# Performance work log

Measured on AMD Instinct MI355X. Metric: run time of the kernel, lower is better.

The kernel has to match this reference:

```python
import jax, jax.numpy as jnp
import numpy as np

B, J, Q, O, H1, H2 = 16384, 12, 7, 5, 128, 128


def _xavier(key, shape):
    fan_in, fan_out = shape[-2], shape[-1]
    limit = float(np.sqrt(6.0 / (fan_in + fan_out)))
    return jax.random.uniform(key, shape, jnp.float32, -limit, limit)


def setup_inputs() -> dict:
    key = jax.random.key(0)
    ks = jax.random.split(key, 8)
    x = jax.random.uniform(ks[0], (B, Q, O), jnp.float32)
    judge_ids = jax.random.randint(ks[1], (B,), 0, J, jnp.int64)
    return {
        "x": x,
        "judge_ids": judge_ids,
        "W1": _xavier(ks[2], (Q, O + 1, H1)),
        "W1_a": _xavier(ks[3], (J, Q, O + 1, H1)),
        "W2": _xavier(ks[4], (H1 + 1, H2)),
        "W2_a": _xavier(ks[5], (J, H1 + 1, H2)),
        "V": _xavier(ks[6], (Q, H2 + 1, O)),
        "V_a": _xavier(ks[7], (J, Q, H2 + 1, O)),
    }


def reference(x, judge_ids, W1, W1_a, W2, W2_a, V, V_a):
    b, q, _ = x.shape
    ones = jnp.ones((b, q, 1), x.dtype)
    # layer 1: per-(judge, question) weights with bias concat
    x_bias = jnp.concatenate([ones, x], axis=2)            # [b,q,O+1]
    W1c = W1[None] + W1_a[judge_ids]                        # [b,q,O+1,H1]
    z1 = jax.nn.sigmoid(jnp.einsum('bqi,bqih->bqh', x_bias, W1c))
    # layer 2: per-judge weights shared across questions
    z1_bias = jnp.concatenate([ones, z1], axis=2)           # [b,q,H1+1]
    W2c = W2[None] + W2_a[judge_ids]                        # [b,H1+1,H2]
    z2 = jax.nn.sigmoid(jnp.einsum('bqi,bih->bqh', z1_bias, W2c))
    # output layer: per-(judge, question) weights -> softmax over options
    z2_bias = jnp.concatenate([ones, z2], axis=2)           # [b,q,H2+1]
    Vc = V[None] + V_a[judge_ids]                           # [b,q,H2+1,O]
    logits = jnp.einsum('bqi,bqio->bqo', z2_bias, Vc)
    return jax.nn.softmax(logits, axis=-1)                  # [b,q,O]
```

## Files before the change

kernel.cpp:

```cpp
#include <hip/hip_runtime.h>
#include <hip/hip_bf16.h>

#define B_TOT 16384
#define NQ 7
#define NO 5

typedef float v4f __attribute__((ext_vector_type(4)));
typedef _Float16 v8h __attribute__((ext_vector_type(8)));

#define WS_W1F  0
#define WS_W2F  (WS_W1F + 49152)
#define WS_V3F  (WS_W2F + 98304)
#define WS_W2L  (WS_V3F + 86016)
#define WS_V3L  (WS_W2L + 1536)
#define WS_PERM (WS_V3L + 1344)
#define WS_HIST (WS_PERM + 12*16384)
#define WS_ISB  (WS_HIST + 768)
#define WS_TOT_U32 (WS_ISB + 1)
#define WS_NEEDED_BYTES ((size_t)WS_TOT_U32 * 4)

#define CFRAG_TOT (49152 + 98304 + 86016 + 1536 + 1344)
#define NBLK_COMBINE ((CFRAG_TOT + 255) / 256)
#define NBLK_SCATTER 64
#define NBLK_PRE (NBLK_COMBINE + NBLK_SCATTER)

__device__ __forceinline__ float ldf(const float* p) { return *p; }
__device__ __forceinline__ float ldf(const __hip_bfloat16* p) { return __bfloat162float(*p); }
__device__ __forceinline__ float sigmoidf_(float v) { return 1.0f / (1.0f + __expf(-v)); }
__device__ __forceinline__ unsigned short f2h(float f) {
    _Float16 h = (_Float16)f; return __builtin_bit_cast(unsigned short, h);
}
__device__ __forceinline__ float h2f(unsigned short u) {
    return (float)__builtin_bit_cast(_Float16, u);
}
__device__ __forceinline__ unsigned pack2(float a, float b) {
    return (unsigned)f2h(a) | ((unsigned)f2h(b) << 16);
}
__device__ __forceinline__ v8h bc8h(uint4 u) { return __builtin_bit_cast(v8h, u); }

__device__ __forceinline__ int probe_is_bf16(const unsigned int* w1bits) {
    int hits = 0;
    for (int t = 0; t < 64; ++t) {
        unsigned lo = w1bits[t] & 0xFFFFu, e = (lo >> 7) & 0xFFu;
        if (lo == 0u || (e >= 100u && e <= 130u)) ++hits;
    }
    return hits >= 32;
}
__device__ __forceinline__ int probe_is_j64(const int* jid) {
    int o = 0;
    for (int t = 0; t < 64; ++t) o |= jid[2*t + 1];
    return (o == 0) ? 1 : 0;
}

template<typename T>
__device__ __forceinline__ void combine_body(
    int idx, const T* W1, const T* W1a, const T* W2, const T* W2a,
    const T* V, const T* Va, unsigned* ws32, float* wsF)
{
    if (idx < 49152) {
        int p = idx & 3, l = (idx >> 2) & 63, nt = (idx >> 8) & 7,
            ks = (idx >> 11) & 1, j = idx >> 12;
        int n = nt*16 + (l & 15);
        float v[2];
        #pragma unroll
        for (int s = 0; s < 2; ++s) {
            int k = ks*32 + ((l >> 4) << 3) + 2*p + s;
            v[s] = (k < 42) ? (ldf(W1 + k*128 + n) + ldf(W1a + j*5376 + k*128 + n)) : 0.0f;
        }
        ws32[WS_W1F + idx] = pack2(v[0], v[1]);
    } else if (idx < 49152 + 98304) {
        int t = idx - 49152;
        int p = t & 3, l = (t >> 2) & 63, nt = (t >> 8) & 7,
            ks = (t >> 11) & 3, j = t >> 13;
        int n = nt*16 + (l & 15);
        float v[2];
        #pragma unroll
        for (int s = 0; s < 2; ++s) {
            int k = ks*32 + ((l >> 4) << 3) + 2*p + s;
            v[s] = ldf(W2 + k*128 + n) + ldf(W2a + (j*129 + k)*128 + n);
        }
        ws32[WS_W2F + t] = pack2(v[0], v[1]);
    } else if (idx < 49152 + 98304 + 86016) {
        int t = idx - (49152 + 98304);
        int p = t & 3, l = (t >> 2) & 63, ks = (t >> 8) & 3;
        int jq = t >> 10, q = jq % 7, j = jq / 7;
        int n = l & 15;
        float v[2];
        #pragma unroll
        for (int s = 0; s < 2; ++s) {
            int k = ks*32 + ((l >> 4) << 3) + 2*p + s;
            v[s] = (n < 5) ? (ldf(V + q*645 + k*5 + n) + ldf(Va + j*4515 + q*645 + k*5 + n))
                           : 0.0f;
        }
        ws32[WS_V3F + t] = pack2(v[0], v[1]);
    } else if (idx < 49152 + 98304 + 86016 + 1536) {
        int t = idx - (49152 + 98304 + 86016);
        int j = t >> 7, n = t & 127;
        wsF[WS_W2L + t] = ldf(W2 + 128*128 + n) + ldf(W2a + (j*129 + 128)*128 + n);
    } else if (idx < CFRAG_TOT) {
        int t = idx - (49152 + 98304 + 86016 + 1536);
        int c = t & 15, jq = t >> 4, q = jq % 7, j = jq / 7;
        wsF[WS_V3L + t] = (c < 5)
            ? (ldf(V + q*645 + 640 + c) + ldf(Va + j*4515 + q*645 + 640 + c)) : 0.0f;
    }
}

__global__ __launch_bounds__(256) void fused_pre_kernel(
    const void* W1, const void* W1a, const void* W2, const void* W2a,
    const void* V,  const void* Va,  const int* jid, unsigned* ws32)
{
    __shared__ int sflag;
    __shared__ int wq[4][12];
    const int tid = threadIdx.x;
    int* wsI = (int*)ws32;

    if ((int)blockIdx.x < NBLK_COMBINE) {
        if (tid < 64) {
            unsigned wb = ((const unsigned*)W1)[tid];
            unsigned lo = wb & 0xFFFFu, e = (lo >> 7) & 0xFFu;
            unsigned long long mb = __ballot(lo == 0u || (e >= 100u && e <= 130u));
            if (tid == 0) sflag = (__popcll(mb) >= 32);
        }
        __syncthreads();
        const int isb = sflag;
        int idx = blockIdx.x * 256 + tid;
        if (idx >= CFRAG_TOT) return;
        float* wsF = (float*)ws32;
        if (isb) combine_body(idx,
            (const __hip_bfloat16*)W1, (const __hip_bfloat16*)W1a,
            (const __hip_bfloat16*)W2, (const __hip_bfloat16*)W2a,
            (const __hip_bfloat16*)V,  (const __hip_bfloat16*)Va, ws32, wsF);
        else combine_body(idx,
            (const float*)W1, (const float*)W1a, (const float*)W2,
            (const float*)W2a, (const float*)V, (const float*)Va, ws32, wsF);
    } else {
        const int sblk = blockIdx.x - NBLK_COMBINE;
        const int l = tid & 63, w = tid >> 6;
        if (sblk == 0 && tid < 64) {
            unsigned wb = ((const unsigned*)W1)[tid];
            unsigned lo = wb & 0xFFFFu, e = (lo >> 7) & 0xFFu;
            unsigned long long mb = __ballot(lo == 0u || (e >= 100u && e <= 130u));
            if (tid == 0) wsI[WS_ISB] = (__popcll(mb) >= 32);
        }
        if (tid < 64) {
            unsigned long long mo = __ballot(jid[2*tid + 1] != 0);
            if (tid == 0) sflag = (mo == 0ULL);
        }
        __syncthreads();
        const int j64 = sflag;
        const int idx = sblk * 256 + tid;
        const int j = j64 ? jid[2*idx] : jid[idx];

        int rloc = 0;
        int c[12];
        #pragma unroll
        for (int jj = 0; jj < 12; ++jj) {
            unsigned long long mk = __ballot(j == jj);
            c[jj] = (int)__popcll(mk);
            if (j == jj) rloc = (int)__popcll(mk & ((1ULL << l) - 1ULL));
        }
        if (l == 0) {
            #pragma unroll
            for (int jj = 0; jj < 12; ++jj) wq[w][jj] = c[jj];
        }
        __syncthreads();
        int pre = 0;
        #pragma unroll
        for (int w2 = 0; w2 < 4; ++w2)
            if (w2 < w) pre += wq[w2][j];
        wsI[WS_PERM + j*16384 + sblk*256 + pre + rloc] = idx;
        if (tid < 12)
            wsI[WS_HIST + sblk*12 + tid] =
                wq[0][tid] + wq[1][tid] + wq[2][tid] + wq[3][tid];
    }
}

#define Z_STRIDE 136
#define A_STRIDE 72
__global__ __launch_bounds__(256) void CalibrationNetwork_81329500717524_kernel(
    const void* xraw, const unsigned* __restrict__ ws32, float* __restrict__ out)
{
    __shared__ __align__(16) unsigned short z1L[112 * Z_STRIDE];
    __shared__ __align__(16) unsigned short z2A[112 * Z_STRIDE];
    __shared__ int pref[12 * 65];
    __shared__ int pvals[16];
    float* lg = (float*)z1L;
    int* histL = (int*)z2A;

    const int* wsI = (const int*)ws32;
    const int tid = threadIdx.x;
    const int l = tid & 63, w = tid >> 6;
    const int quad = l >> 4, m = l & 15;
    const int isb = wsI[WS_ISB];

    for (int i = tid; i < 768; i += 256) histL[i] = wsI[WS_HIST + i];
    __syncthreads();
    #pragma unroll
    for (int jo = 0; jo < 3; ++jo) {
        const int j = w*3 + jo;
        int vc = histL[l*12 + j];
        int s = vc;
        #pragma unroll
        for (int off = 1; off < 64; off <<= 1) {
            int t = __shfl_up(s, off, 64);
            if (l >= off) s += t;
        }
        pref[j*65 + l] = s - vc;
        if (l == 63) pref[j*65 + 64] = s;
    }
    __syncthreads();
    int cntR[12];
    #pragma unroll
    for (int jj = 0; jj < 12; ++jj) cntR[jj] = pref[jj*65 + 64];
    int totTiles = 0;
    #pragma unroll
    for (int jj = 0; jj < 12; ++jj) totTiles += (cntR[jj] + 15) >> 4;

    #pragma unroll 1
    for (int v = blockIdx.x; v < totTiles; v += gridDim.x) {
        int jT = 0, tT = 0, cj = 0, acc = 0;
        #pragma unroll
        for (int jj = 0; jj < 12; ++jj) {
            int c = cntR[jj], nt = (c + 15) >> 4;
            if (v >= acc && v < acc + nt) { jT = jj; tT = v - acc; cj = c; }
            acc += nt;
        }
        const int valid = min(16, cj - tT*16);

        __syncthreads();

        {
            uint4 zz; zz.x = 0; zz.y = 0; zz.z = 0; zz.w = 0;
            uint4* a128 = (uint4*)z2A;
            for (int i = tid; i < 112 * A_STRIDE / 8; i += 256) a128[i] = zz;
            if (tid < 112) z1L[tid * Z_STRIDE] = 0x3C00;
            if (tid < 16) {
                int bl = tid < valid ? tid : valid - 1;
                int r = tT*16 + bl;
                int k = 0;
                #pragma unroll
                for (int kk = 1; kk < 64; ++kk)
                    if (pref[jT*65 + kk] <= r) k = kk;
                pvals[tid] = wsI[WS_PERM + jT*16384 + k*256 + (r - pref[jT*65 + k])];
            }
        }
        __syncthreads();
        if (tid < 112) {
            int bl = tid / 7, q = tid - bl*7;
            int bg = pvals[bl];
            float x0, x1, x2, x3, x4;
            if (isb) {
                const __hip_bfloat16* xp = (const __hip_bfloat16*)xraw + bg*35 + q*5;
                x0 = ldf(xp); x1 = ldf(xp+1); x2 = ldf(xp+2); x3 = ldf(xp+3); x4 = ldf(xp+4);
            } else {
                const float* xp = (const float*)xraw + bg*35 + q*5;
                x0 = xp[0]; x1 = xp[1]; x2 = xp[2]; x3 = xp[3]; x4 = xp[4];
            }
            unsigned* rp = (unsigned*)&z2A[tid * A_STRIDE + q*6];
            rp[0] = 0x3C00u | ((unsigned)f2h(x0) << 16);
            rp[1] = pack2(x1, x2);
            rp[2] = pack2(x3, x4);
        }
        __syncthreads();

        {
            const uint4* BF = (const uint4*)(ws32 + WS_W1F) + jT*1024;
            #pragma unroll
            for (int nt2 = 0; nt2 < 2; ++nt2) {
                const int nt = w*2 + nt2;
                const uint4 b0 = BF[(0*8 + nt)*64 + l];
                const uint4 b1 = BF[(1*8 + nt)*64 + l];
                #pragma unroll 1
                for (int mt = 0; mt < 7; ++mt) {
                    const uint4 a0 = *(const uint4*)&z2A[(mt*16 + m)*A_STRIDE + quad*8];
                    const uint4 a1 = *(const uint4*)&z2A[(mt*16 + m)*A_STRIDE + 32 + quad*8];
                    v4f acc2 = {0.f, 0.f, 0.f, 0.f};
                    acc2 = __builtin_amdgcn_mfma_f32_16x16x32_f16(bc8h(a0), bc8h(b0), acc2, 0, 0, 0);
                    acc2 = __builtin_amdgcn_mfma_f32_16x16x32_f16(bc8h(a1), bc8h(b1), acc2, 0, 0, 0);
                    const int col = nt*16 + m;
                    #pragma unroll
                    for (int i = 0; i < 4; ++i) {
                        int row = mt*16 + quad*4 + i;
                        z1L[row*Z_STRIDE + 1 + col] = f2h(sigmoidf_(acc2[i]));
                    }
                }
            }
        }
        __syncthreads();

        {
            if (tid < 112) z2A[tid * Z_STRIDE] = 0x3C00;
            const uint4* BF = (const uint4*)(ws32 + WS_W2F) + jT*2048;
            const float* w2l = (const float*)ws32 + WS_W2L + jT*128;
            #pragma unroll
            for (int nt2 = 0; nt2 < 2; ++nt2) {
                const int nt = w*2 + nt2;
                uint4 Bv[4];
                #pragma unroll
                for (int ks = 0; ks < 4; ++ks) Bv[ks] = BF[(ks*8 + nt)*64 + l];
                const float wl = w2l[nt*16 + m];
                #pragma unroll 1
                for (int mt = 0; mt < 7; ++mt) {
                    v4f acc2 = {0.f, 0.f, 0.f, 0.f};
                    #pragma unroll
                    for (int ks = 0; ks < 4; ++ks) {
                        const uint4 a = *(const uint4*)&z1L[(mt*16 + m)*Z_STRIDE + ks*32 + quad*8];
                        acc2 = __builtin_amdgcn_mfma_f32_16x16x32_f16(bc8h(a), bc8h(Bv[ks]), acc2, 0, 0, 0);
                    }
                    const int col = nt*16 + m;
                    #pragma unroll
                    for (int i = 0; i < 4; ++i) {
                        int row = mt*16 + quad*4 + i;
                        float zl = h2f(z1L[row*Z_STRIDE + 128]);
                        float vv = acc2[i] + zl * wl;
                        z2A[row*Z_STRIDE + 1 + col] = f2h(sigmoidf_(vv));
                    }
                }
            }
        }
        __syncthreads();

        {
            const uint4* BF = (const uint4*)(ws32 + WS_V3F) + jT*7*256;
            const float* v3l = (const float*)ws32 + WS_V3L + jT*7*16;
            #pragma unroll 1
            for (int qi = 0; qi < 2; ++qi) {
                const int q = w + qi*4;
                if (q > 6) break;
                v4f acc2 = {0.f, 0.f, 0.f, 0.f};
                #pragma unroll
                for (int ks = 0; ks < 4; ++ks) {
                    const uint4 b = BF[q*256 + ks*64 + l];
                    const uint4 a = *(const uint4*)&z2A[(m*7 + q)*Z_STRIDE + ks*32 + quad*8];
                    acc2 = __builtin_amdgcn_mfma_f32_16x16x32_f16(bc8h(a), bc8h(b), acc2, 0, 0, 0);
                }
                const float vl = v3l[q*16 + m];
                #pragma unroll
                for (int i = 0; i < 4; ++i) {
                    int bloc = quad*4 + i;
                    float zl = h2f(z2A[(bloc*7 + q)*Z_STRIDE + 128]);
                    float logit = acc2[i] + zl * vl;
                    if (m < 5) lg[(bloc*7 + q)*8 + m] = logit;
                }
            }
        }
        __syncthreads();

        if (tid < 112) {
            int bl = tid / 7, q = tid - bl*7;
            const float* pr = &lg[tid*8];
            float p0 = pr[0], p1 = pr[1], p2 = pr[2], p3 = pr[3], p4 = pr[4];
            float mx = fmaxf(fmaxf(fmaxf(p0, p1), fmaxf(p2, p3)), p4);
            float e0 = __expf(p0 - mx), e1 = __expf(p1 - mx), e2 = __expf(p2 - mx),
                  e3 = __expf(p3 - mx), e4 = __expf(p4 - mx);
            float inv = 1.0f / (e0 + e1 + e2 + e3 + e4);
            if (bl < valid) {
                float* op = out + (size_t)pvals[bl]*35 + q*5;
                op[0] = e0*inv; op[1] = e1*inv; op[2] = e2*inv; op[3] = e3*inv; op[4] = e4*inv;
            }
        }
    }
}

template<typename T>
__device__ void direct_body(
    const T* __restrict__ x, const int* __restrict__ jid, int j64,
    const T* __restrict__ W1, const T* __restrict__ W1a,
    const T* __restrict__ W2, const T* __restrict__ W2a,
    const T* __restrict__ V,  const T* __restrict__ Va,
    float* __restrict__ out, float (*lds_z1)[NQ][128])
{
    const int tid = threadIdx.x;
    const int l = tid & 63, w = tid >> 6;
    #pragma unroll 1
    for (int t = 0; t < 4; ++t) {
        const int b = blockIdx.x * 16 + w * 4 + t;
        const int j = j64 ? jid[2*b] : jid[b];
        float xv = 0.0f;
        if (l < 35) xv = ldf(x + b*35 + l);
        #pragma unroll
        for (int q = 0; q < NQ; ++q) {
            const T* Wq  = W1  + q*768;
            const T* Waq = W1a + j*5376 + q*768;
            float a  = ldf(Wq + l)      + ldf(Waq + l);
            float bb = ldf(Wq + 64 + l) + ldf(Waq + 64 + l);
            #pragma unroll
            for (int i = 1; i <= 5; ++i) {
                float xi = __shfl(xv, q*5 + (i - 1), 64);
                a  = fmaf(xi, ldf(Wq + i*128 + l)      + ldf(Waq + i*128 + l),      a);
                bb = fmaf(xi, ldf(Wq + i*128 + 64 + l) + ldf(Waq + i*128 + 64 + l), bb);
            }
            lds_z1[w][q][l]      = sigmoidf_(a);
            lds_z1[w][q][64 + l] = sigmoidf_(bb);
        }
        __syncthreads();
        float accA[NQ], accB[NQ];
        {
            const float biasA = ldf(W2 + l)      + ldf(W2a + j*129*128 + l);
            const float biasB = ldf(W2 + 64 + l) + ldf(W2a + j*129*128 + 64 + l);
            #pragma unroll
            for (int q = 0; q < NQ; ++q) { accA[q] = biasA; accB[q] = biasB; }
        }
        #pragma unroll 1
        for (int k = 0; k < 128; ++k) {
            const int i = k + 1;
            const float wA = ldf(W2 + i*128 + l)      + ldf(W2a + (j*129 + i)*128 + l);
            const float wB = ldf(W2 + i*128 + 64 + l) + ldf(W2a + (j*129 + i)*128 + 64 + l);
            #pragma unroll
            for (int q = 0; q < NQ; ++q) {
                const float z = lds_z1[w][q][k];
                accA[q] = fmaf(wA, z, accA[q]);
                accB[q] = fmaf(wB, z, accB[q]);
            }
        }
        __syncthreads();
        #pragma unroll 1
        for (int q = 0; q < NQ; ++q) {
            const float zA = sigmoidf_(accA[q]);
            const float zB = sigmoidf_(accB[q]);
            const T* Vq  = V  + q*645;
            const T* Vaq = Va + j*4515 + q*645;
            float p[NO];
            #pragma unroll
            for (int o = 0; o < NO; ++o) {
                float vA = ldf(Vq + (1 + l)*5 + o)  + ldf(Vaq + (1 + l)*5 + o);
                float vB = ldf(Vq + (65 + l)*5 + o) + ldf(Vaq + (65 + l)*5 + o);
                p[o] = zA*vA + zB*vB;
            }
            #pragma unroll
            for (int off = 32; off > 0; off >>= 1) {
                #pragma unroll
                for (int o = 0; o < NO; ++o) p[o] += __shfl_xor(p[o], off, 64);
            }
            #pragma unroll
            for (int o = 0; o < NO; ++o) p[o] += ldf(Vq + o) + ldf(Vaq + o);
            float mx = fmaxf(fmaxf(fmaxf(p[0], p[1]), fmaxf(p[2], p[3])), p[4]);
            float e[NO], s = 0.0f;
            #pragma unroll
            for (int o = 0; o < NO; ++o) { e[o] = __expf(p[o] - mx); s += e[o]; }
            float inv = 1.0f / s;
            if (l < 5) out[b*35 + q*5 + l] = e[l] * inv;
        }
    }
}

__global__ __launch_bounds__(256) void calib_direct_kernel(
    const void* x, const int* jid,
    const void* W1, const void* W1a, const void* W2, const void* W2a,
    const void* V,  const void* Va, float* out)
{
    __shared__ __align__(16) float lds_z1[4][NQ][128];
    const int isb = probe_is_bf16((const unsigned int*)W1);
    const int j64 = probe_is_j64(jid);
    if (isb) direct_body(
        (const __hip_bfloat16*)x, jid, j64,
        (const __hip_bfloat16*)W1, (const __hip_bfloat16*)W1a,
        (const __hip_bfloat16*)W2, (const __hip_bfloat16*)W2a,
        (const __hip_bfloat16*)V,  (const __hip_bfloat16*)Va, out, lds_z1);
    else direct_body(
        (const float*)x, jid, j64,
        (const float*)W1, (const float*)W1a, (const float*)W2,
        (const float*)W2a, (const float*)V, (const float*)Va, out, lds_z1);
}

extern "C" void kernel_launch(void* const* d_in, const int* in_sizes, int n_in,
                              void* d_out, int out_size, void* d_ws, size_t ws_size,
                              hipStream_t stream)
{
    const void* x   = d_in[0];
    const int*  jid = (const int*)d_in[1];
    const void* W1  = d_in[2];
    const void* W1a = d_in[3];
    const void* W2  = d_in[4];
    const void* W2a = d_in[5];
    const void* V   = d_in[6];
    const void* Va  = d_in[7];
    float* out = (float*)d_out;

    if (ws_size >= WS_NEEDED_BYTES) {
        unsigned* ws32 = (unsigned*)d_ws;
        fused_pre_kernel<<<NBLK_PRE, 256, 0, stream>>>(
            W1, W1a, W2, W2a, V, Va, jid, ws32);
        CalibrationNetwork_81329500717524_kernel<<<512, 256, 0, stream>>>(
            x, ws32, out);
    } else {
        calib_direct_kernel<<<B_TOT / 16, 256, 0, stream>>>(
            x, jid, W1, W1a, W2, W2a, V, Va, out);
    }
}
```

Before: 107.3 us.

## Halve per-tile batch to 8 samples and double grid size

Each tile now covers 8 batch rows instead of 16 (56 question rows padded to 64 instead of 112), and the grid doubles to 1024 blocks. Shared memory per block drops and the M-tile loops shrink from 7 to 4, which is meant to raise occupancy, cut the tail padding per judge group, and give the GPU more parallel tiles. The input staging now builds each padded row in registers and writes it with vector stores instead of zeroing the buffer first. In exchange, each block reloads the per-judge weight fragments for half as much work, and the output layer still issues full 16-row MFMAs with half the rows duplicated.

Result: faster. 104.9 us, median of 2 (-2.2%).

```diff
diff --git a/kernel.cpp b/kernel.cpp
--- a/kernel.cpp
+++ b/kernel.cpp
@@ -180,10 +180,10 @@
 __global__ __launch_bounds__(256) void CalibrationNetwork_81329500717524_kernel(
     const void* xraw, const unsigned* __restrict__ ws32, float* __restrict__ out)
 {
-    __shared__ __align__(16) unsigned short z1L[112 * Z_STRIDE];
-    __shared__ __align__(16) unsigned short z2A[112 * Z_STRIDE];
+    __shared__ __align__(16) unsigned short z1L[64 * Z_STRIDE];
+    __shared__ __align__(16) unsigned short z2A[64 * Z_STRIDE];
     __shared__ int pref[12 * 65];
-    __shared__ int pvals[16];
+    __shared__ int pvals[8];
     float* lg = (float*)z1L;
     int* histL = (int*)z2A;
 
@@ -214,52 +214,58 @@
     for (int jj = 0; jj < 12; ++jj) cntR[jj] = pref[jj*65 + 64];
     int totTiles = 0;
     #pragma unroll
-    for (int jj = 0; jj < 12; ++jj) totTiles += (cntR[jj] + 15) >> 4;
+    for (int jj = 0; jj < 12; ++jj) totTiles += (cntR[jj] + 7) >> 3;
 
     #pragma unroll 1
     for (int v = blockIdx.x; v < totTiles; v += gridDim.x) {
         int jT = 0, tT = 0, cj = 0, acc = 0;
         #pragma unroll
         for (int jj = 0; jj < 12; ++jj) {
-            int c = cntR[jj], nt = (c + 15) >> 4;
+            int c = cntR[jj], nt = (c + 7) >> 3;
             if (v >= acc && v < acc + nt) { jT = jj; tT = v - acc; cj = c; }
             acc += nt;
         }
-        const int valid = min(16, cj - tT*16);
-
-        __syncthreads();
-
-        {
-            uint4 zz; zz.x = 0; zz.y = 0; zz.z = 0; zz.w = 0;
-            uint4* a128 = (uint4*)z2A;
-            for (int i = tid; i < 112 * A_STRIDE / 8; i += 256) a128[i] = zz;
-            if (tid < 112) z1L[tid * Z_STRIDE] = 0x3C00;
-            if (tid < 16) {
-                int bl = tid < valid ? tid : valid - 1;
-                int r = tT*16 + bl;
-                int k = 0;
-                #pragma unroll
-                for (int kk = 1; kk < 64; ++kk)
-                    if (pref[jT*65 + kk] <= r) k = kk;
-                pvals[tid] = wsI[WS_PERM + jT*16384 + k*256 + (r - pref[jT*65 + k])];
-            }
-        }
-        __syncthreads();
-        if (tid < 112) {
-            int bl = tid / 7, q = tid - bl*7;
-            int bg = pvals[bl];
-            float x0, x1, x2, x3, x4;
-            if (isb) {
-                const __hip_bfloat16* xp = (const __hip_bfloat16*)xraw + bg*35 + q*5;
-                x0 = ldf(xp); x1 = ldf(xp+1); x2 = ldf(xp+2); x3 = ldf(xp+3); x4 = ldf(xp+4);
-            } else {
-                const float* xp = (const float*)xraw + bg*35 + q*5;
-                x0 = xp[0]; x1 = xp[1]; x2 = xp[2]; x3 = xp[3]; x4 = xp[4];
-            }
-            unsigned* rp = (unsigned*)&z2A[tid * A_STRIDE + q*6];
-            rp[0] = 0x3C00u | ((unsigned)f2h(x0) << 16);
-            rp[1] = pack2(x1, x2);
-            rp[2] = pack2(x3, x4);
+        const int valid = min(8, cj - tT*8);
+
+        __syncthreads();
+
+        if (tid < 64) z1L[tid * Z_STRIDE] = 0x3C00;
+        if (tid < 8) {
+            int bl = tid < valid ? tid : valid - 1;
+            int r = tT*8 + bl;
+            int k = 0;
+            #pragma unroll
+            for (int kk = 1; kk < 64; ++kk)
+                if (pref[jT*65 + kk] <= r) k = kk;
+            pvals[tid] = wsI[WS_PERM + jT*16384 + k*256 + (r - pref[jT*65 + k])];
+        }
+        __syncthreads();
+        if (tid < 64) {
+            unsigned wbuf[32];
+            #pragma unroll
+            for (int i = 0; i < 32; ++i) wbuf[i] = 0u;
+            if (tid < 56) {
+                int bl = tid / 7, q = tid - bl*7;
+                int bg = pvals[bl];
+                float x0, x1, x2, x3, x4;
+                if (isb) {
+                    const __hip_bfloat16* xp = (const __hip_bfloat16*)xraw + bg*35 + q*5;
+                    x0 = ldf(xp); x1 = ldf(xp+1); x2 = ldf(xp+2); x3 = ldf(xp+3); x4 = ldf(xp+4);
+                } else {
+                    const float* xp = (const float*)xraw + bg*35 + q*5;
+                    x0 = xp[0]; x1 = xp[1]; x2 = xp[2]; x3 = xp[3]; x4 = xp[4];
+                }
+                wbuf[q*3]     = 0x3C00u | ((unsigned)f2h(x0) << 16);
+                wbuf[q*3 + 1] = pack2(x1, x2);
+                wbuf[q*3 + 2] = pack2(x3, x4);
+            }
+            uint4* rowp = (uint4*)&z2A[tid * A_STRIDE];
+            #pragma unroll
+            for (int i = 0; i < 8; ++i) {
+                uint4 u; u.x = wbuf[4*i]; u.y = wbuf[4*i+1];
+                u.z = wbuf[4*i+2]; u.w = wbuf[4*i+3];
+                rowp[i] = u;
+            }
         }
         __syncthreads();
 
@@ -271,7 +277,7 @@
                 const uint4 b0 = BF[(0*8 + nt)*64 + l];
                 const uint4 b1 = BF[(1*8 + nt)*64 + l];
                 #pragma unroll 1
-                for (int mt = 0; mt < 7; ++mt) {
+                for (int mt = 0; mt < 4; ++mt) {
                     const uint4 a0 = *(const uint4*)&z2A[(mt*16 + m)*A_STRIDE + quad*8];
                     const uint4 a1 = *(const uint4*)&z2A[(mt*16 + m)*A_STRIDE + 32 + quad*8];
                     v4f acc2 = {0.f, 0.f, 0.f, 0.f};
@@ -289,7 +295,7 @@
         __syncthreads();
 
         {
-            if (tid < 112) z2A[tid * Z_STRIDE] = 0x3C00;
+            if (tid < 64) z2A[tid * Z_STRIDE] = 0x3C00;
             const uint4* BF = (const uint4*)(ws32 + WS_W2F) + jT*2048;
             const float* w2l = (const float*)ws32 + WS_W2L + jT*128;
             #pragma unroll
@@ -300,7 +306,7 @@
                 for (int ks = 0; ks < 4; ++ks) Bv[ks] = BF[(ks*8 + nt)*64 + l];
                 const float wl = w2l[nt*16 + m];
                 #pragma unroll 1
-                for (int mt = 0; mt < 7; ++mt) {
+                for (int mt = 0; mt < 4; ++mt) {
                     v4f acc2 = {0.f, 0.f, 0.f, 0.f};
                     #pragma unroll
                     for (int ks = 0; ks < 4; ++ks) {
@@ -327,26 +333,28 @@
             for (int qi = 0; qi < 2; ++qi) {
                 const int q = w + qi*4;
                 if (q > 6) break;
+                const int mrow = (m & 7)*7 + q;
                 v4f acc2 = {0.f, 0.f, 0.f, 0.f};
                 #pragma unroll
                 for (int ks = 0; ks < 4; ++ks) {
                     const uint4 b = BF[q*256 + ks*64 + l];
-                    const uint4 a = *(const uint4*)&z2A[(m*7 + q)*Z_STRIDE + ks*32 + quad*8];
+                    const uint4 a = *(const uint4*)&z2A[mrow*Z_STRIDE + ks*32 + quad*8];
                     acc2 = __builtin_amdgcn_mfma_f32_16x16x32_f16(bc8h(a), bc8h(b), acc2, 0, 0, 0);
                 }
                 const float vl = v3l[q*16 + m];
                 #pragma unroll
                 for (int i = 0; i < 4; ++i) {
                     int bloc = quad*4 + i;
-                    float zl = h2f(z2A[(bloc*7 + q)*Z_STRIDE + 128]);
-                    float logit = acc2[i] + zl * vl;
-                    if (m < 5) lg[(bloc*7 + q)*8 + m] = logit;
+                    if (bloc < 8 && m < 5) {
+                        float zl = h2f(z2A[(bloc*7 + q)*Z_STRIDE + 128]);
+                        lg[(bloc*7 + q)*8 + m] = acc2[i] + zl * vl;
+                    }
                 }
             }
         }
         __syncthreads();
 
-        if (tid < 112) {
+        if (tid < 56) {
             int bl = tid / 7, q = tid - bl*7;
             const float* pr = &lg[tid*8];
             float p0 = pr[0], p1 = pr[1], p2 = pr[2], p3 = pr[3], p4 = pr[4];
@@ -481,7 +489,7 @@
         unsigned* ws32 = (unsigned*)d_ws;
         fused_pre_kernel<<<NBLK_PRE, 256, 0, stream>>>(
             W1, W1a, W2, W2a, V, Va, jid, ws32);
-        CalibrationNetwork_81329500717524_kernel<<<512, 256, 0, stream>>>(
+        CalibrationNetwork_81329500717524_kernel<<<1024, 256, 0, stream>>>(
             x, ws32, out);
     } else {
         calib_direct_kernel<<<B_TOT / 16, 256, 0, stream>>>(
```
